# Kernel tuning notes

Hardware: AMD Instinct MI355X
Metric: run time of the kernel (lower is better)

Reference implementation:

```python
import jax, jax.numpy as jnp
import numpy as np


def setup_inputs() -> dict:
    key = jax.random.key(0)
    k1, k2, *kw = jax.random.split(key, 12)
    N, E = 10000, 320000
    D_IN, D_HID, D_EMB, D_PRED = 2, 128, 256, 128

    def lin(k, fan_in, fan_out):
        bound = 1.0 / np.sqrt(fan_in)
        kw_, kb_ = jax.random.split(k)
        W = jax.random.uniform(kw_, (fan_in, fan_out), jnp.float32, -bound, bound)
        b = jax.random.uniform(kb_, (fan_out,), jnp.float32, -bound, bound)
        return W, b

    W1, b1 = lin(kw[0], D_IN, D_HID)
    W2, b2 = lin(kw[1], D_HID, D_EMB)
    Wp1, bp1 = lin(kw[2], D_EMB, D_PRED)
    Wp2, bp2 = lin(kw[3], D_PRED, 1)

    src = jax.random.randint(k1, (E,), 0, N, dtype=jnp.int32)
    dst = jax.random.randint(k2, (E,), 0, N, dtype=jnp.int32)
    return {
        "W1": W1, "b1": b1, "W2": W2, "b2": b2,
        "Wp1": Wp1, "bp1": bp1, "Wp2": Wp2, "bp2": bp2,
        "src": src, "dst": dst, "num_nodes": N,
    }


def reference(W1, b1, W2, b2, Wp1, bp1, Wp2, bp2, src, dst, num_nodes):
    N = num_nodes
    E = src.shape[0]
    ones = jnp.ones((E,), jnp.float32)
    # node features = [in_degree, out_degree]  -> [N, 2]
    in_deg = jax.ops.segment_sum(ones, dst, num_segments=N)
    out_deg = jax.ops.segment_sum(ones, src, num_segments=N)
    x = jnp.stack([in_deg, out_deg], axis=1)

    def gcn_agg(h):
        # sum of messages from source nodes into destination nodes (SpMM-like)
        return jax.ops.segment_sum(h[src], dst, num_segments=N)

    h = jax.nn.relu(gcn_agg(x) @ W1 + b1)        # [N, 128]
    h = gcn_agg(h) @ W2 + b2                     # [N, 256]
    h = jax.nn.relu(h)
    graph_embedding = jnp.sum(h, axis=0)         # [256] (dgl.sum_nodes, single graph)
    m = jax.nn.relu(graph_embedding @ Wp1 + bp1)
    metric = m @ Wp2 + bp2                       # [1]
    return (graph_embedding, metric)
```

## Files before the change

kernel.cpp:

```cpp
#include <hip/hip_runtime.h>

#define N_NODES 10000
#define CAPLOG 7
#define CAP 128
#define NPART 16
#define NBH 128
#define TBH 512
#define TSTRIDE 132
#define HB 128

__global__ __launch_bounds__(TBH) void hist_kernel(const int* __restrict__ src,
                                                   const int* __restrict__ dst,
                                                   unsigned int* __restrict__ cnt,
                                                   float* __restrict__ ge_p,
                                                   float* __restrict__ m,
                                                   unsigned int* __restrict__ done,
                                                   int E) {
  __shared__ unsigned int hist[N_NODES];
  const int tid = threadIdx.x, bid = blockIdx.x;
  for (int i = tid; i < N_NODES; i += TBH) hist[i] = 0;
  if (bid < NPART && tid < 256) ge_p[(bid << 8) + tid] = 0.f;
  if (bid == NPART && tid < HB) m[tid] = 0.f;
  if (bid == NPART && tid == HB) *done = 0u;
  __syncthreads();
  const int chunk = (E + NBH - 1) / NBH;
  const int e0 = bid * chunk, e1 = min(E, e0 + chunk);
  for (int e = e0 + tid; e < e1; e += TBH) {
    atomicAdd(&hist[dst[e]], 1u);
    atomicAdd(&hist[src[e]], 0x10000u);
  }
  __syncthreads();
  unsigned int* outb = cnt + (size_t)bid * N_NODES;
  for (int i = tid; i < N_NODES; i += TBH) outb[i] = hist[i];
}

__global__ __launch_bounds__(256) void scan_kernel(const unsigned int* __restrict__ cnt,
                                                   unsigned int* __restrict__ off,
                                                   unsigned int* __restrict__ pack) {
  const int n = blockIdx.x * 256 + threadIdx.x;
  if (n >= N_NODES) return;
  unsigned run = 0;
#pragma unroll 8
  for (int b = 0; b < NBH; ++b) {
    unsigned v = cnt[(size_t)b * N_NODES + n];
    off[(size_t)b * N_NODES + n] = run;
    run += v;
  }
  pack[n] = run;
}

__global__ __launch_bounds__(TBH) void scatter_kernel(const int* __restrict__ src,
                                                      const int* __restrict__ dst,
                                                      const unsigned int* __restrict__ off,
                                                      unsigned short* __restrict__ slots,
                                                      int E) {
  __shared__ unsigned int cur[N_NODES];
  const int tid = threadIdx.x, bid = blockIdx.x;
  const unsigned int* ob = off + (size_t)bid * N_NODES;
  for (int i = tid; i < N_NODES; i += TBH) cur[i] = ob[i];
  __syncthreads();
  const int chunk = (E + NBH - 1) / NBH;
  const int e0 = bid * chunk, e1 = min(E, e0 + chunk);
  for (int e = e0 + tid; e < e1; e += TBH) {
    int d = dst[e];
    unsigned idx = atomicAdd(&cur[d], 1u) & 0xFFFFu;
    if (idx < CAP) slots[(d << CAPLOG) + idx] = (unsigned short)src[e];
  }
}

__global__ __launch_bounds__(256) void agg1_kernel(const unsigned int* __restrict__ pack,
                                                   const unsigned short* __restrict__ slots,
                                                   unsigned int* __restrict__ a) {
  const int tid = threadIdx.x;
  const int hw = tid >> 5, hl = tid & 31;
  const int node = blockIdx.x * 8 + hw;
  const int deg = min((int)(pack[node] & 0xFFFFu), CAP);
  const int base = node << CAPLOG;
  unsigned acc = 0u;
  for (int e = hl; e < deg; e += 32) acc += pack[slots[base + e]];
#pragma unroll
  for (int off = 16; off > 0; off >>= 1) acc += (unsigned)__shfl_xor((int)acc, off, 32);
  if (hl == 0) a[node] = acc;
}

#define FMA_ROW(aR0, aR1, aR2, aR3, t)                                       \
  aR0 = fmaf(t.x, w0.x, aR0); aR0 = fmaf(t.y, w1.x, aR0);                    \
  aR0 = fmaf(t.z, w2v.x, aR0); aR0 = fmaf(t.w, w3.x, aR0);                   \
  aR1 = fmaf(t.x, w0.y, aR1); aR1 = fmaf(t.y, w1.y, aR1);                    \
  aR1 = fmaf(t.z, w2v.y, aR1); aR1 = fmaf(t.w, w3.y, aR1);                   \
  aR2 = fmaf(t.x, w0.z, aR2); aR2 = fmaf(t.y, w1.z, aR2);                    \
  aR2 = fmaf(t.z, w2v.z, aR2); aR2 = fmaf(t.w, w3.z, aR2);                   \
  aR3 = fmaf(t.x, w0.w, aR3); aR3 = fmaf(t.y, w1.w, aR3);                    \
  aR3 = fmaf(t.z, w2v.w, aR3); aR3 = fmaf(t.w, w3.w, aR3);

__global__ __launch_bounds__(256, 4) void agg2gemm2_kernel(const unsigned int* __restrict__ pack,
                                                           const unsigned short* __restrict__ slots,
                                                           const unsigned int* __restrict__ a,
                                                           const float* __restrict__ W1,
                                                           const float* __restrict__ b1,
                                                           const float* __restrict__ W2,
                                                           const float* __restrict__ b2,
                                                           float* __restrict__ ge_p) {
  __shared__ float2 s_a[16][CAP + 1];
  __shared__ float s_t[16 * TSTRIDE];
  __shared__ float s_red[4][256];
  const int tid = threadIdx.x, bid = blockIdx.x;
  const int hw = tid >> 5, hl = tid & 31;

#pragma unroll
  for (int nn = 0; nn < 2; ++nn) {
    const int row = hw * 2 + nn;
    const int node = bid * 16 + row;
    const int deg = min((int)(pack[node] & 0xFFFFu), CAP);
    const int base = node << CAPLOG;
    for (int e = hl; e < deg; e += 32) {
      const unsigned v = a[slots[base + e]];
      s_a[row][e] = make_float2((float)(v & 0xFFFFu), (float)(v >> 16));
    }
  }

  float w10[4], w11[4], bb[4];
#pragma unroll
  for (int c = 0; c < 4; ++c) {
    w10[c] = W1[4 * hl + c];
    w11[c] = W1[128 + 4 * hl + c];
    bb[c] = b1[4 * hl + c];
  }
  __syncthreads();

#pragma unroll
  for (int nn = 0; nn < 2; ++nn) {
    const int row = hw * 2 + nn;
    const int node = bid * 16 + row;
    const int deg = min((int)(pack[node] & 0xFFFFu), CAP);
    float acc0 = 0.f, acc1 = 0.f, acc2 = 0.f, acc3 = 0.f;
#pragma unroll 4
    for (int j = 0; j < deg; ++j) {
      const float2 av = s_a[row][j];
      acc0 += fmaxf(fmaf(av.x, w10[0], fmaf(av.y, w11[0], bb[0])), 0.f);
      acc1 += fmaxf(fmaf(av.x, w10[1], fmaf(av.y, w11[1], bb[1])), 0.f);
      acc2 += fmaxf(fmaf(av.x, w10[2], fmaf(av.y, w11[2], bb[2])), 0.f);
      acc3 += fmaxf(fmaf(av.x, w10[3], fmaf(av.y, w11[3], bb[3])), 0.f);
    }
    float* tr = s_t + row * TSTRIDE + 4 * hl;
    tr[0] = acc0; tr[1] = acc1; tr[2] = acc2; tr[3] = acc3;
  }
  __syncthreads();

  const int jq = tid & 63, ng = tid >> 6;
  const int j = jq << 2;
  const float* tb = s_t + (ng << 2) * TSTRIDE;
  float4 wc0 = *(const float4*)(W2 + 0 * 256 + j);
  float4 wc1 = *(const float4*)(W2 + 1 * 256 + j);
  float4 wc2 = *(const float4*)(W2 + 2 * 256 + j);
  float4 wc3 = *(const float4*)(W2 + 3 * 256 + j);
  float a00 = 0.f, a01 = 0.f, a02 = 0.f, a03 = 0.f;
  float a10 = 0.f, a11 = 0.f, a12 = 0.f, a13 = 0.f;
  float a20 = 0.f, a21 = 0.f, a22 = 0.f, a23 = 0.f;
  float a30 = 0.f, a31 = 0.f, a32 = 0.f, a33 = 0.f;
#pragma unroll 4
  for (int k = 0; k < 124; k += 4) {
    const float4 wn0 = *(const float4*)(W2 + (k + 4) * 256 + j);
    const float4 wn1 = *(const float4*)(W2 + (k + 5) * 256 + j);
    const float4 wn2 = *(const float4*)(W2 + (k + 6) * 256 + j);
    const float4 wn3 = *(const float4*)(W2 + (k + 7) * 256 + j);
    const float4 t0 = *(const float4*)(tb + 0 * TSTRIDE + k);
    const float4 t1 = *(const float4*)(tb + 1 * TSTRIDE + k);
    const float4 t2 = *(const float4*)(tb + 2 * TSTRIDE + k);
    const float4 t3 = *(const float4*)(tb + 3 * TSTRIDE + k);
    {
      const float4 w0 = wc0, w1 = wc1, w2v = wc2, w3 = wc3;
      FMA_ROW(a00, a01, a02, a03, t0)
      FMA_ROW(a10, a11, a12, a13, t1)
      FMA_ROW(a20, a21, a22, a23, t2)
      FMA_ROW(a30, a31, a32, a33, t3)
    }
    wc0 = wn0; wc1 = wn1; wc2 = wn2; wc3 = wn3;
  }
  {
    const float4 t0 = *(const float4*)(tb + 0 * TSTRIDE + 124);
    const float4 t1 = *(const float4*)(tb + 1 * TSTRIDE + 124);
    const float4 t2 = *(const float4*)(tb + 2 * TSTRIDE + 124);
    const float4 t3 = *(const float4*)(tb + 3 * TSTRIDE + 124);
    const float4 w0 = wc0, w1 = wc1, w2v = wc2, w3 = wc3;
    FMA_ROW(a00, a01, a02, a03, t0)
    FMA_ROW(a10, a11, a12, a13, t1)
    FMA_ROW(a20, a21, a22, a23, t2)
    FMA_ROW(a30, a31, a32, a33, t3)
  }

  const float4 bj = *(const float4*)(b2 + j);
  float4 part;
  part.x = fmaxf(a00 + bj.x, 0.f) + fmaxf(a10 + bj.x, 0.f) +
           fmaxf(a20 + bj.x, 0.f) + fmaxf(a30 + bj.x, 0.f);
  part.y = fmaxf(a01 + bj.y, 0.f) + fmaxf(a11 + bj.y, 0.f) +
           fmaxf(a21 + bj.y, 0.f) + fmaxf(a31 + bj.y, 0.f);
  part.z = fmaxf(a02 + bj.z, 0.f) + fmaxf(a12 + bj.z, 0.f) +
           fmaxf(a22 + bj.z, 0.f) + fmaxf(a32 + bj.z, 0.f);
  part.w = fmaxf(a03 + bj.w, 0.f) + fmaxf(a13 + bj.w, 0.f) +
           fmaxf(a23 + bj.w, 0.f) + fmaxf(a33 + bj.w, 0.f);
  *(float4*)(&s_red[ng][j]) = part;
  __syncthreads();
  const float g = (s_red[0][tid] + s_red[1][tid]) + (s_red[2][tid] + s_red[3][tid]);
  atomicAdd(&ge_p[((bid & (NPART - 1)) << 8) + tid], g);
}

__global__ __launch_bounds__(256) void head_kernel(const float* __restrict__ ge_p,
                                                   const float* __restrict__ Wp1,
                                                   const float* __restrict__ bp1,
                                                   const float* __restrict__ Wp2,
                                                   const float* __restrict__ bp2,
                                                   float* __restrict__ m,
                                                   unsigned int* __restrict__ done,
                                                   float* __restrict__ out) {
  __shared__ float s_r[4];
  __shared__ int s_last;
  const int tid = threadIdx.x, j = blockIdx.x;
  float g = 0.f;
#pragma unroll
  for (int p = 0; p < NPART; ++p) g += ge_p[p * 256 + tid];
  if (j == 0) out[tid] = g;
  float part = g * Wp1[tid * 128 + j];
#pragma unroll
  for (int o = 32; o > 0; o >>= 1) part += __shfl_xor(part, o);
  if ((tid & 63) == 0) s_r[tid >> 6] = part;
  __syncthreads();
  if (tid == 0) {
    const float mj = bp1[j] + (s_r[0] + s_r[1]) + (s_r[2] + s_r[3]);
    atomicAdd(&m[j], mj);
    __threadfence();
    s_last = (atomicAdd(done, 1u) == HB - 1) ? 1 : 0;
  }
  __syncthreads();
  if (!s_last) return;
  float v = 0.f;
  if (tid < 128)
    v = fmaxf(__hip_atomic_load(&m[tid], __ATOMIC_RELAXED, __HIP_MEMORY_SCOPE_AGENT), 0.f) *
        Wp2[tid];
#pragma unroll
  for (int o = 32; o > 0; o >>= 1) v += __shfl_xor(v, o);
  if ((tid & 63) == 0) s_r[tid >> 6] = v;
  __syncthreads();
  if (tid == 0) out[256] = s_r[0] + s_r[1] + bp2[0];
}

extern "C" void kernel_launch(void* const* d_in, const int* in_sizes, int n_in,
                              void* d_out, int out_size, void* d_ws, size_t ws_size,
                              hipStream_t stream) {
  const float* W1 = (const float*)d_in[0];
  const float* b1 = (const float*)d_in[1];
  const float* W2 = (const float*)d_in[2];
  const float* b2 = (const float*)d_in[3];
  const float* Wp1 = (const float*)d_in[4];
  const float* bp1 = (const float*)d_in[5];
  const float* Wp2 = (const float*)d_in[6];
  const float* bp2 = (const float*)d_in[7];
  const int* src = (const int*)d_in[8];
  const int* dst = (const int*)d_in[9];
  const int E = in_sizes[8];
  const int N = N_NODES;

  char* p = (char*)d_ws;
  float* ge_p = (float*)p;               p += (size_t)NPART * 256 * 4;
  float* m = (float*)p;                  p += HB * 4;
  unsigned int* done = (unsigned int*)p; p += 16;
  unsigned int* pack = (unsigned int*)p; p += (size_t)N * 4;
  unsigned int* a = (unsigned int*)p;    p += (size_t)N * 4;
  unsigned short* slots = (unsigned short*)p; p += (size_t)N * CAP * 2;
  unsigned int* cnt = (unsigned int*)p;  p += (size_t)NBH * N * 4;
  unsigned int* off = (unsigned int*)p;
  float* out = (float*)d_out;

  hist_kernel<<<NBH, TBH, 0, stream>>>(src, dst, cnt, ge_p, m, done, E);
  scan_kernel<<<(N + 255) / 256, 256, 0, stream>>>(cnt, off, pack);
  scatter_kernel<<<NBH, TBH, 0, stream>>>(src, dst, off, slots, E);
  agg1_kernel<<<N / 8, 256, 0, stream>>>(pack, slots, a);
  agg2gemm2_kernel<<<N / 16, 256, 0, stream>>>(pack, slots, a, W1, b1, W2, b2, ge_p);
  head_kernel<<<HB, 256, 0, stream>>>(ge_p, Wp1, bp1, Wp2, bp2, m, done, out);
}
```

Baseline: 129.4 us.

## Parallelize scan with shared-memory tiles and deepen W2 prefetch in GEMM

The scan kernel now loads a 128x64 tile of per-block histogram counts into shared memory. It splits each node column's 128-entry prefix sum across four thread groups with a two-level scan, which raises block count and parallelism over the old one-thread-per-node serial loop. The agg2gemm2 GEMM loop now prefetches W2 rows two iterations ahead instead of one, to hide global load latency. This costs more registers and shared memory per block, which could reduce occupancy.

```diff
diff --git a/kernel.cpp b/kernel.cpp
--- a/kernel.cpp
+++ b/kernel.cpp
@@ -8,6 +8,7 @@
 #define TBH 512
 #define TSTRIDE 132
 #define HB 128
+#define SNB 64
 
 __global__ __launch_bounds__(TBH) void hist_kernel(const int* __restrict__ src,
                                                    const int* __restrict__ dst,
@@ -37,16 +38,38 @@
 __global__ __launch_bounds__(256) void scan_kernel(const unsigned int* __restrict__ cnt,
                                                    unsigned int* __restrict__ off,
                                                    unsigned int* __restrict__ pack) {
-  const int n = blockIdx.x * 256 + threadIdx.x;
-  if (n >= N_NODES) return;
+  __shared__ unsigned int tile[NBH][SNB + 1];
+  __shared__ unsigned int qsum[4][SNB + 1];
+  const int tid = threadIdx.x;
+  const int n0 = blockIdx.x * SNB;
+  for (int i = tid; i < NBH * SNB; i += 256) {
+    const int b = i >> 6, n = i & (SNB - 1);
+    const int gn = n0 + n;
+    tile[b][n] = (gn < N_NODES) ? cnt[(size_t)b * N_NODES + gn] : 0u;
+  }
+  __syncthreads();
+  const int q = tid >> 6, n = tid & (SNB - 1);
   unsigned run = 0;
-#pragma unroll 8
-  for (int b = 0; b < NBH; ++b) {
-    unsigned v = cnt[(size_t)b * N_NODES + n];
-    off[(size_t)b * N_NODES + n] = run;
-    run += v;
-  }
-  pack[n] = run;
+#pragma unroll
+  for (int j = 0; j < 32; ++j) run += tile[(q << 5) + j][n];
+  qsum[q][n] = run;
+  __syncthreads();
+  unsigned base = 0;
+  for (int p = 0; p < q; ++p) base += qsum[p][n];
+  unsigned r = base;
+#pragma unroll
+  for (int j = 0; j < 32; ++j) {
+    const unsigned v = tile[(q << 5) + j][n];
+    tile[(q << 5) + j][n] = r;
+    r += v;
+  }
+  if (q == 3 && n0 + n < N_NODES) pack[n0 + n] = r;
+  __syncthreads();
+  for (int i = tid; i < NBH * SNB; i += 256) {
+    const int b = i >> 6, nn = i & (SNB - 1);
+    const int gn = n0 + nn;
+    if (gn < N_NODES) off[(size_t)b * N_NODES + gn] = tile[b][nn];
+  }
 }
 
 __global__ __launch_bounds__(TBH) void scatter_kernel(const int* __restrict__ src,
@@ -92,6 +115,19 @@
   aR2 = fmaf(t.z, w2v.z, aR2); aR2 = fmaf(t.w, w3.z, aR2);                   \
   aR3 = fmaf(t.x, w0.w, aR3); aR3 = fmaf(t.y, w1.w, aR3);                    \
   aR3 = fmaf(t.z, w2v.w, aR3); aR3 = fmaf(t.w, w3.w, aR3);
+
+#define COMPUTE_GROUP(kk, W0, W1, W2V, W3)                                   \
+  {                                                                          \
+    const float4 t0 = *(const float4*)(tb + 0 * TSTRIDE + (kk));             \
+    const float4 t1 = *(const float4*)(tb + 1 * TSTRIDE + (kk));             \
+    const float4 t2 = *(const float4*)(tb + 2 * TSTRIDE + (kk));             \
+    const float4 t3 = *(const float4*)(tb + 3 * TSTRIDE + (kk));             \
+    const float4 w0 = W0, w1 = W1, w2v = W2V, w3 = W3;                       \
+    FMA_ROW(a00, a01, a02, a03, t0)                                          \
+    FMA_ROW(a10, a11, a12, a13, t1)                                          \
+    FMA_ROW(a20, a21, a22, a23, t2)                                          \
+    FMA_ROW(a30, a31, a32, a33, t3)                                          \
+  }
 
 __global__ __launch_bounds__(256, 4) void agg2gemm2_kernel(const unsigned int* __restrict__ pack,
                                                            const unsigned short* __restrict__ slots,
@@ -150,44 +186,31 @@
   const int jq = tid & 63, ng = tid >> 6;
   const int j = jq << 2;
   const float* tb = s_t + (ng << 2) * TSTRIDE;
-  float4 wc0 = *(const float4*)(W2 + 0 * 256 + j);
-  float4 wc1 = *(const float4*)(W2 + 1 * 256 + j);
-  float4 wc2 = *(const float4*)(W2 + 2 * 256 + j);
-  float4 wc3 = *(const float4*)(W2 + 3 * 256 + j);
+  const float* w2p = W2 + j;
+  float4 wc0 = *(const float4*)(w2p + 0 * 256);
+  float4 wc1 = *(const float4*)(w2p + 1 * 256);
+  float4 wc2 = *(const float4*)(w2p + 2 * 256);
+  float4 wc3 = *(const float4*)(w2p + 3 * 256);
+  float4 wn0 = *(const float4*)(w2p + 4 * 256);
+  float4 wn1 = *(const float4*)(w2p + 5 * 256);
+  float4 wn2 = *(const float4*)(w2p + 6 * 256);
+  float4 wn3 = *(const float4*)(w2p + 7 * 256);
   float a00 = 0.f, a01 = 0.f, a02 = 0.f, a03 = 0.f;
   float a10 = 0.f, a11 = 0.f, a12 = 0.f, a13 = 0.f;
   float a20 = 0.f, a21 = 0.f, a22 = 0.f, a23 = 0.f;
   float a30 = 0.f, a31 = 0.f, a32 = 0.f, a33 = 0.f;
-#pragma unroll 4
-  for (int k = 0; k < 124; k += 4) {
-    const float4 wn0 = *(const float4*)(W2 + (k + 4) * 256 + j);
-    const float4 wn1 = *(const float4*)(W2 + (k + 5) * 256 + j);
-    const float4 wn2 = *(const float4*)(W2 + (k + 6) * 256 + j);
-    const float4 wn3 = *(const float4*)(W2 + (k + 7) * 256 + j);
-    const float4 t0 = *(const float4*)(tb + 0 * TSTRIDE + k);
-    const float4 t1 = *(const float4*)(tb + 1 * TSTRIDE + k);
-    const float4 t2 = *(const float4*)(tb + 2 * TSTRIDE + k);
-    const float4 t3 = *(const float4*)(tb + 3 * TSTRIDE + k);
-    {
-      const float4 w0 = wc0, w1 = wc1, w2v = wc2, w3 = wc3;
-      FMA_ROW(a00, a01, a02, a03, t0)
-      FMA_ROW(a10, a11, a12, a13, t1)
-      FMA_ROW(a20, a21, a22, a23, t2)
-      FMA_ROW(a30, a31, a32, a33, t3)
-    }
+#pragma unroll 5
+  for (int k = 0; k < 120; k += 4) {
+    const float4 wm0 = *(const float4*)(w2p + (k + 8) * 256);
+    const float4 wm1 = *(const float4*)(w2p + (k + 9) * 256);
+    const float4 wm2 = *(const float4*)(w2p + (k + 10) * 256);
+    const float4 wm3 = *(const float4*)(w2p + (k + 11) * 256);
+    COMPUTE_GROUP(k, wc0, wc1, wc2, wc3)
     wc0 = wn0; wc1 = wn1; wc2 = wn2; wc3 = wn3;
-  }
-  {
-    const float4 t0 = *(const float4*)(tb + 0 * TSTRIDE + 124);
-    const float4 t1 = *(const float4*)(tb + 1 * TSTRIDE + 124);
-    const float4 t2 = *(const float4*)(tb + 2 * TSTRIDE + 124);
-    const float4 t3 = *(const float4*)(tb + 3 * TSTRIDE + 124);
-    const float4 w0 = wc0, w1 = wc1, w2v = wc2, w3 = wc3;
-    FMA_ROW(a00, a01, a02, a03, t0)
-    FMA_ROW(a10, a11, a12, a13, t1)
-    FMA_ROW(a20, a21, a22, a23, t2)
-    FMA_ROW(a30, a31, a32, a33, t3)
-  }
+    wn0 = wm0; wn1 = wm1; wn2 = wm2; wn3 = wm3;
+  }
+  COMPUTE_GROUP(120, wc0, wc1, wc2, wc3)
+  COMPUTE_GROUP(124, wn0, wn1, wn2, wn3)
 
   const float4 bj = *(const float4*)(b2 + j);
   float4 part;
@@ -272,7 +295,7 @@
   float* out = (float*)d_out;
 
   hist_kernel<<<NBH, TBH, 0, stream>>>(src, dst, cnt, ge_p, m, done, E);
-  scan_kernel<<<(N + 255) / 256, 256, 0, stream>>>(cnt, off, pack);
+  scan_kernel<<<(N + SNB - 1) / SNB, 256, 0, stream>>>(cnt, off, pack);
   scatter_kernel<<<NBH, TBH, 0, stream>>>(src, dst, off, slots, E);
   agg1_kernel<<<N / 8, 256, 0, stream>>>(pack, slots, a);
   agg2gemm2_kernel<<<N / 16, 256, 0, stream>>>(pack, slots, a, W1, b1, W2, b2, ge_p);
```

Measured after the change: 133.9 us. +3.5%, slower.
